# Kernel tuning notes

Hardware: AMD Instinct MI355X
Metric: run time of the kernel (lower is better)

The kernel has to match this reference:

```python
import jax, jax.numpy as jnp
import numpy as np

N = 100000
E = 1600000
DIN = 165
DH = 128


def setup_inputs() -> dict:
    key = jax.random.key(0)
    ks = jax.random.split(key, 10)
    def nrm(k, shape, scale=0.1):
        return jax.random.normal(k, shape, dtype=jnp.float32) * scale
    x = jax.random.normal(ks[0], (N, DIN), dtype=jnp.float32)
    edge_index = jax.random.randint(ks[1], (2, E), 0, N, dtype=jnp.int64)
    return dict(
        x=x,
        edge_index=edge_index,
        fb_w1=nrm(ks[2], (DIN, DIN // 2)),
        fb_w2=nrm(ks[3], (DIN // 2, DIN)),
        sage_wl=nrm(ks[4], (DIN, DH)),
        sage_bl=jnp.zeros((DH,), jnp.float32),
        sage_wr=nrm(ks[5], (DIN, DH)),
        gat_w=nrm(ks[6], (DH, DH // 2)),
        gat_att_src=nrm(ks[7], (DH // 2,)),
        gat_att_dst=nrm(ks[8], (DH // 2,)),
        gat_b=jnp.zeros((DH // 2,), jnp.float32),
        cheb_w=nrm(ks[9], (DH // 2, 1)),
        cheb_b=jnp.zeros((1,), jnp.float32),
    )


def _segment_softmax(logits, seg, num_segments):
    mx = jax.ops.segment_max(logits, seg, num_segments=num_segments)
    e = jnp.exp(logits - mx[seg])
    s = jax.ops.segment_sum(e, seg, num_segments=num_segments)
    return e / (s[seg] + 1e-16)


def reference(x, edge_index, fb_w1, fb_w2, sage_wl, sage_bl, sage_wr,
              gat_w, gat_att_src, gat_att_dst, gat_b, cheb_w, cheb_b):
    n = x.shape[0]
    src, dst = edge_index[0], edge_index[1]

    # FeatureBooster: scatter over batch=arange(n) is identity for max and sum,
    # so max_result == sum_result == x and y = sigmoid(mlp(x) + mlp(x)).
    m = jnp.maximum(x @ fb_w1, 0.0) @ fb_w2
    x = x * jax.nn.sigmoid(m + m)

    # SAGEConv (mean aggregation): out = lin_l(mean_agg(x_src -> dst)) + lin_r(x)
    agg = jax.ops.segment_sum(x[src], dst, num_segments=n)  # [n, DIN]
    cnt = jax.ops.segment_sum(jnp.ones((src.shape[0],), x.dtype), dst, num_segments=n)
    agg = agg / jnp.maximum(cnt, 1.0)[:, None]
    x = agg @ sage_wl + sage_bl + x @ sage_wr
    x = jnp.maximum(x, 0.0)  # relu; dropout is identity in eval mode

    # GATConv (heads=1) with default add_self_loops=True
    ar = jnp.arange(n, dtype=src.dtype)
    si = jnp.concatenate([src, ar])
    di = jnp.concatenate([dst, ar])
    h = x @ gat_w                      # [n, 64]
    a_s = h @ gat_att_src              # [n]
    a_d = h @ gat_att_dst              # [n]
    e = a_s[si] + a_d[di]
    e = jnp.where(e > 0, e, 0.2 * e)   # leaky_relu slope 0.2
    alpha = _segment_softmax(e, di, n)
    x = jax.ops.segment_sum(h[si] * alpha[:, None], di, num_segments=n) + gat_b
    x = jnp.maximum(x, 0.0)

    # ChebConv with K=1: T_0(x) = x, so it's a plain linear layer.
    x = x @ cheb_w + cheb_b
    return jax.nn.sigmoid(x)
```

## Files before the change

kernel.cpp:

```cpp
#include <hip/hip_runtime.h>
#include <hip/hip_bf16.h>

#define N_NODES 100000
#define N_EDGES 1600000
#define DIN 165
#define DHID 82
#define DH 128
#define DG 64

typedef _Float16 f16;
typedef f16 f16x8 __attribute__((ext_vector_type(8)));
typedef f16 f16x4 __attribute__((ext_vector_type(4)));
typedef f16 f16x2 __attribute__((ext_vector_type(2)));
typedef float f32x4 __attribute__((ext_vector_type(4)));

#define MFMA16(a, b, c) __builtin_amdgcn_mfma_f32_16x16x32_f16(a, b, c, 0, 0, 0)


__global__ __launch_bounds__(256) void rank_xpad_kernel(const float* __restrict__ x,
                                                        f16* __restrict__ Xp,
                                                        const int* __restrict__ dst,
                                                        int* __restrict__ cnt,
                                                        int* __restrict__ rank) {
    int gid = blockIdx.x * 256 + threadIdx.x;
    if (gid < N_EDGES) rank[gid] = atomicAdd(&cnt[dst[gid]], 1);
    int node = gid / 48, g = gid % 48;
    int col0 = g * 4;
    f16x4 o;
#pragma unroll
    for (int j = 0; j < 4; j++) {
        int c = col0 + j;
        o[j] = (f16)((c < DIN) ? x[(long)node * DIN + c] : 0.f);
    }
    *((f16x4*)(Xp + (long)node * 192 + col0)) = o;
}

__global__ __launch_bounds__(1024) void scan1_kernel(const int* __restrict__ cnt,
                                                     int* __restrict__ rowptr,
                                                     int* __restrict__ bsum) {
    __shared__ int wsum[16];
    int tid = threadIdx.x, lane = tid & 63, wid = tid >> 6;
    int i = blockIdx.x * 1024 + tid;
    int v = (i < N_NODES) ? cnt[i] : 0;
    int xv = v;
#pragma unroll
    for (int off = 1; off < 64; off <<= 1) {
        int t = __shfl_up(xv, off);
        if (lane >= off) xv += t;
    }
    if (lane == 63) wsum[wid] = xv;
    __syncthreads();
    if (wid == 0 && lane < 16) {
        int wv = wsum[lane];
#pragma unroll
        for (int off = 1; off < 16; off <<= 1) {
            int t = __shfl_up(wv, off);
            if (lane >= off) wv += t;
        }
        wsum[lane] = wv;
    }
    __syncthreads();
    int off0 = wid ? wsum[wid - 1] : 0;
    if (i < N_NODES) rowptr[i] = off0 + xv - v;
    if (tid == 1023) bsum[blockIdx.x] = off0 + xv;
}

__global__ __launch_bounds__(64) void scan2_kernel(const int* __restrict__ bsum,
                                                   int* __restrict__ boff,
                                                   int* __restrict__ rowptr,
                                                   int nblocks) {
    int lane = threadIdx.x;
    int c = 0;
    for (int base = 0; base < nblocks; base += 64) {
        int idx = base + lane;
        int v = (idx < nblocks) ? bsum[idx] : 0;
        int xv = v;
#pragma unroll
        for (int off = 1; off < 64; off <<= 1) {
            int t = __shfl_up(xv, off);
            if (lane >= off) xv += t;
        }
        if (idx < nblocks) boff[idx] = c + xv - v;
        c += __shfl(xv, 63);
    }
    if (lane == 0) rowptr[N_NODES] = c;
}

__global__ __launch_bounds__(1024) void scan3_kernel(int* __restrict__ rowptr,
                                                     const int* __restrict__ boff) {
    int i = blockIdx.x * 1024 + threadIdx.x;
    if (i < N_NODES) rowptr[i] += boff[blockIdx.x];
}

__global__ __launch_bounds__(256) void h_fill_kernel(const f16* __restrict__ Xp,
                                                     const float* __restrict__ w1,
                                                     f16* __restrict__ H,
                                                     const int* __restrict__ src,
                                                     const int* __restrict__ dst,
                                                     const int* __restrict__ rank,
                                                     const int* __restrict__ rowptr,
                                                     int* __restrict__ esrc) {
    int tid = threadIdx.x, wave = tid >> 6, lane = tid & 63;
    {
        int tg = blockIdx.x * 256 + tid;
        for (int e = tg; e < N_EDGES; e += 384 * 256) {
            int d = dst[e];
            __builtin_nontemporal_store(src[e], &esrc[rowptr[d] + rank[e]]);
        }
    }
    int q = lane >> 4, l16 = lane & 15;
    int blk = blockIdx.x;
    int g = (blk >> 3) & 1;
    int chunk = (blk & 7) + 8 * (blk >> 4);
    int nbase = g * 48;
    f16x8 bf[3][6];
#pragma unroll
    for (int nt = 0; nt < 3; nt++) {
        int col = nbase + nt * 16 + l16;
#pragma unroll
        for (int ks = 0; ks < 6; ks++) {
            int kb = ks * 32 + q * 8;
            f16x8 b;
#pragma unroll
            for (int j = 0; j < 8; j++) {
                int k = kb + j;
                b[j] = (f16)((k < DIN && col < DHID) ? w1[k * DHID + col] : 0.f);
            }
            bf[nt][ks] = b;
        }
    }
    for (int mt = chunk * 4 + wave; mt < 6250; mt += 768) {
        const f16* xr = Xp + (long)(mt * 16 + l16) * 192;
        f32x4 acc[3];
#pragma unroll
        for (int nt = 0; nt < 3; nt++) acc[nt] = (f32x4){0.f, 0.f, 0.f, 0.f};
#pragma unroll
        for (int ks = 0; ks < 6; ks++) {
            f16x8 a = *((const f16x8*)(xr + ks * 32 + q * 8));
#pragma unroll
            for (int nt = 0; nt < 3; nt++) acc[nt] = MFMA16(a, bf[nt][ks], acc[nt]);
        }
#pragma unroll
        for (int nt = 0; nt < 3; nt++) {
            int col = nbase + nt * 16 + l16;
#pragma unroll
            for (int r = 0; r < 4; r++) {
                int node = mt * 16 + q * 4 + r;
                H[(long)node * 96 + col] = (f16)fmaxf(acc[nt][r], 0.f);
            }
        }
    }
}

__global__ __launch_bounds__(256) void y_kernel(const f16* __restrict__ Xp,
                                                const f16* __restrict__ H,
                                                const float* __restrict__ w2,
                                                f16* __restrict__ Y) {
    int tid = threadIdx.x, wave = tid >> 6, lane = tid & 63;
    int q = lane >> 4, l16 = lane & 15;
    int blk = blockIdx.x;
    int g = (blk >> 3) & 3;
    int chunk = (blk & 7) + 8 * (blk >> 5);
    int nbase = g * 48;
    f16x8 bf[3][3];
#pragma unroll
    for (int nt = 0; nt < 3; nt++) {
        int col = nbase + nt * 16 + l16;
#pragma unroll
        for (int ks = 0; ks < 3; ks++) {
            int kb = ks * 32 + q * 8;
            f16x8 b;
#pragma unroll
            for (int j = 0; j < 8; j++) {
                int k = kb + j;
                b[j] = (f16)((k < DHID && col < DIN) ? w2[k * DIN + col] : 0.f);
            }
            bf[nt][ks] = b;
        }
    }
    for (int mt = chunk * 4 + wave; mt < 6250; mt += 768) {
        const f16* hr = H + (long)(mt * 16 + l16) * 96;
        f32x4 acc[3];
#pragma unroll
        for (int nt = 0; nt < 3; nt++) acc[nt] = (f32x4){0.f, 0.f, 0.f, 0.f};
#pragma unroll
        for (int ks = 0; ks < 3; ks++) {
            f16x8 a = *((const f16x8*)(hr + ks * 32 + q * 8));
#pragma unroll
            for (int nt = 0; nt < 3; nt++) acc[nt] = MFMA16(a, bf[nt][ks], acc[nt]);
        }
#pragma unroll
        for (int nt = 0; nt < 3; nt++) {
            int col = nbase + nt * 16 + l16;
#pragma unroll
            for (int r = 0; r < 4; r++) {
                int node = mt * 16 + q * 4 + r;
                float gg = 1.f / (1.f + __expf(-2.f * acc[nt][r]));
                float xv = (float)Xp[(long)node * 192 + col];
                Y[(long)node * 192 + col] = (f16)(xv * gg);
            }
        }
    }
}

__global__ __launch_bounds__(256) void sage_lin_kernel(const f16* __restrict__ Y,
                                                       const float* __restrict__ wl,
                                                       const float* __restrict__ wr,
                                                       const float* __restrict__ bl,
                                                       f16* __restrict__ t_l,
                                                       f16* __restrict__ x2) {
    int tid = threadIdx.x, wave = tid >> 6, lane = tid & 63;
    int q = lane >> 4, l16 = lane & 15;
    int blk = blockIdx.x;
    int g = (blk >> 3) & 3;
    int chunk = (blk & 7) + 8 * (blk >> 5);
    bool isR = (g >= 2);
    const float* W = isR ? wr : wl;
    int cbase = (g & 1) * 64;
    f16x8 bf[4][6];
    float blv[4];
#pragma unroll
    for (int nt = 0; nt < 4; nt++) {
        int col = cbase + nt * 16 + l16;
        blv[nt] = isR ? bl[col] : 0.f;
#pragma unroll
        for (int ks = 0; ks < 6; ks++) {
            int kb = ks * 32 + q * 8;
            f16x8 b;
#pragma unroll
            for (int j = 0; j < 8; j++) {
                int k = kb + j;
                b[j] = (f16)((k < DIN) ? W[k * DH + col] : 0.f);
            }
            bf[nt][ks] = b;
        }
    }
    for (int mt = chunk * 4 + wave; mt < 6250; mt += 768) {
        const f16* yrow = Y + (long)(mt * 16 + l16) * 192;
        f32x4 acc[4];
#pragma unroll
        for (int nt = 0; nt < 4; nt++) acc[nt] = (f32x4){0.f, 0.f, 0.f, 0.f};
#pragma unroll
        for (int ks = 0; ks < 6; ks++) {
            f16x8 a = *((const f16x8*)(yrow + ks * 32 + q * 8));
#pragma unroll
            for (int nt = 0; nt < 4; nt++) acc[nt] = MFMA16(a, bf[nt][ks], acc[nt]);
        }
#pragma unroll
        for (int nt = 0; nt < 4; nt++) {
            int col = cbase + nt * 16 + l16;
#pragma unroll
            for (int r = 0; r < 4; r++) {
                int node = mt * 16 + q * 4 + r;
                if (isR)
                    x2[(long)node * DH + col] = (f16)(acc[nt][r] + blv[nt]);
                else
                    t_l[(long)node * DH + col] = (f16)acc[nt][r];
            }
        }
    }
}

__global__ __launch_bounds__(256) void sage_agg_kernel(const f16* __restrict__ t_l,
                                                       const int* __restrict__ rowptr,
                                                       const int* __restrict__ esrc,
                                                       f16* __restrict__ x2) {
    int wid = threadIdx.x >> 6, lane = threadIdx.x & 63;
    int i = blockIdx.x * 4 + wid;
    int r0 = rowptr[i], r1 = rowptr[i + 1];
    int quarter = lane >> 4, fq = lane & 15;
    float acc[8];
#pragma unroll
    for (int k = 0; k < 8; k++) acc[k] = 0.f;
    for (int e0 = r0; e0 < r1; e0 += 64) {
        int cnt = min(64, r1 - e0);
        int sn_v = (lane < cnt) ? esrc[e0 + lane] : 0;
        int jmax = (cnt + 3) >> 2;
        for (int j = 0; j < jmax; j++) {
            int idx = 4 * j + quarter;
            int sn = __shfl(sn_v, idx);
            float v = (idx < cnt) ? 1.f : 0.f;
            f16x8 p = *((const f16x8*)(t_l + ((long)sn << 7) + fq * 8));
#pragma unroll
            for (int k = 0; k < 8; k++) acc[k] = fmaf(v, (float)p[k], acc[k]);
        }
    }
#pragma unroll
    for (int k = 0; k < 8; k++) {
        acc[k] += __shfl_xor(acc[k], 16);
        acc[k] += __shfl_xor(acc[k], 32);
    }
    if (quarter == 0) {
        float inv = 1.f / fmaxf((float)(r1 - r0), 1.f);
        f16x8* xp = (f16x8*)(x2 + (long)i * DH + fq * 8);
        f16x8 pre = *xp;
        f16x8 o;
#pragma unroll
        for (int k = 0; k < 8; k++) o[k] = (f16)fmaxf((float)pre[k] + acc[k] * inv, 0.f);
        *xp = o;
    }
}

__global__ __launch_bounds__(256) void gat_h_kernel(const f16* __restrict__ x2,
                                                    const float* __restrict__ gw,
                                                    const float* __restrict__ att_s_w,
                                                    const float* __restrict__ att_d_w,
                                                    f16* __restrict__ h,
                                                    float* __restrict__ a_s,
                                                    float* __restrict__ a_d) {
    int tid = threadIdx.x, wave = tid >> 6, lane = tid & 63;
    int q = lane >> 4, l16 = lane & 15;
    f16x8 bf[4][4];
    float asw[4], adw[4];
#pragma unroll
    for (int nt = 0; nt < 4; nt++) {
        int col = nt * 16 + l16;
        asw[nt] = att_s_w[col];
        adw[nt] = att_d_w[col];
#pragma unroll
        for (int ks = 0; ks < 4; ks++) {
            int kb = ks * 32 + q * 8;
            f16x8 b;
#pragma unroll
            for (int j = 0; j < 8; j++) b[j] = (f16)gw[(kb + j) * DG + col];
            bf[nt][ks] = b;
        }
    }
    int stride = gridDim.x * 4;
    for (int mt = blockIdx.x * 4 + wave; mt < 6250; mt += stride) {
        const f16* xr = x2 + (long)(mt * 16 + l16) * DH;
        f32x4 acc[4];
#pragma unroll
        for (int nt = 0; nt < 4; nt++) acc[nt] = (f32x4){0.f, 0.f, 0.f, 0.f};
#pragma unroll
        for (int ks = 0; ks < 4; ks++) {
            f16x8 a = *((const f16x8*)(xr + ks * 32 + q * 8));
#pragma unroll
            for (int nt = 0; nt < 4; nt++) acc[nt] = MFMA16(a, bf[nt][ks], acc[nt]);
        }
#pragma unroll
        for (int r = 0; r < 4; r++) {
            int node = mt * 16 + q * 4 + r;
            float vs = 0.f, vd = 0.f;
#pragma unroll
            for (int nt = 0; nt < 4; nt++) {
                float hv = acc[nt][r];
                h[(long)node * DG + nt * 16 + l16] = (f16)hv;
                vs += hv * asw[nt];
                vd += hv * adw[nt];
            }
#pragma unroll
            for (int off = 1; off < 16; off <<= 1) {
                vs += __shfl_xor(vs, off);
                vd += __shfl_xor(vd, off);
            }
            if (l16 == 0) {
                a_s[node] = vs;
                a_d[node] = vd;
            }
        }
    }
}

__device__ __forceinline__ float leaky02(float v) { return v > 0.f ? v : 0.2f * v; }

__global__ __launch_bounds__(256) void gat_agg_kernel(const f16* __restrict__ h,
                                                      const float* __restrict__ a_s,
                                                      const float* __restrict__ a_d,
                                                      const int* __restrict__ rowptr,
                                                      const int* __restrict__ esrc,
                                                      const float* __restrict__ gat_b,
                                                      const float* __restrict__ cheb_w,
                                                      const float* __restrict__ cheb_b,
                                                      float* __restrict__ out) {
    int wid = threadIdx.x >> 6, lane = threadIdx.x & 63;
    int i = blockIdx.x * 4 + wid;
    int r0 = rowptr[i], r1 = rowptr[i + 1];
    int quarter = lane >> 4, fq = lane & 15;
    float adi = a_d[i];
    float acc[4] = {0.f, 0.f, 0.f, 0.f};
    float sv = 0.f;
    for (int e0 = r0; e0 < r1; e0 += 64) {
        int cnt = min(64, r1 - e0);
        int sn_v = (lane < cnt) ? esrc[e0 + lane] : 0;
        float ev = 0.f;
        if (lane < cnt) ev = __expf(leaky02(a_s[sn_v] + adi));
        sv += ev;
        int jmax = (cnt + 3) >> 2;
        for (int j = 0; j < jmax; j++) {
            int idx = 4 * j + quarter;
            int sn = __shfl(sn_v, idx);
            float w = __shfl(ev, idx);
            f16x4 p = *((const f16x4*)(h + ((long)sn << 6) + fq * 4));
#pragma unroll
            for (int k = 0; k < 4; k++) acc[k] = fmaf(w, (float)p[k], acc[k]);
        }
    }
#pragma unroll
    for (int off = 32; off > 0; off >>= 1) sv += __shfl_xor(sv, off);
#pragma unroll
    for (int k = 0; k < 4; k++) {
        acc[k] += __shfl_xor(acc[k], 16);
        acc[k] += __shfl_xor(acc[k], 32);
    }
    if (quarter == 0) {
        float wself = __expf(leaky02(a_s[i] + adi));
        float s = sv + wself;
        f16x4 ph = *((const f16x4*)(h + ((long)i << 6) + fq * 4));
        float4 gb = ((const float4*)gat_b)[fq];
        float4 cw = ((const float4*)cheb_w)[fq];
        float gbv[4] = {gb.x, gb.y, gb.z, gb.w};
        float cwv[4] = {cw.x, cw.y, cw.z, cw.w};
        float inv = 1.f / s;
        float z = 0.f;
#pragma unroll
        for (int k = 0; k < 4; k++) {
            float o = fmaxf(fmaf(wself, (float)ph[k], acc[k]) * inv + gbv[k], 0.f);
            z = fmaf(o, cwv[k], z);
        }
#pragma unroll
        for (int off = 8; off > 0; off >>= 1) z += __shfl_xor(z, off);
        if (fq == 0) out[i] = 1.f / (1.f + __expf(-(z + cheb_b[0])));
    }
}

extern "C" void kernel_launch(void* const* d_in, const int* in_sizes, int n_in,
                              void* d_out, int out_size, void* d_ws, size_t ws_size,
                              hipStream_t stream) {
    const float* x       = (const float*)d_in[0];
    const int*   eidx    = (const int*)d_in[1];
    const float* fb_w1   = (const float*)d_in[2];
    const float* fb_w2   = (const float*)d_in[3];
    const float* sage_wl = (const float*)d_in[4];
    const float* sage_bl = (const float*)d_in[5];
    const float* sage_wr = (const float*)d_in[6];
    const float* gat_w   = (const float*)d_in[7];
    const float* att_src = (const float*)d_in[8];
    const float* att_dst = (const float*)d_in[9];
    const float* gat_b   = (const float*)d_in[10];
    const float* cheb_w  = (const float*)d_in[11];
    const float* cheb_b  = (const float*)d_in[12];

    const int* src = eidx;
    const int* dst = eidx + N_EDGES;

    char* base = (char*)d_ws;
    f16* Xp = (f16*)base;
    f16* H  = (f16*)(base + 38400000);
    f16* Y  = (f16*)(base + 57600000);
    f16* t_l = (f16*)base;
    f16* x2  = (f16*)(base + 25600000);
    f16* h   = Y;
    float* a_s = (float*)(base + 70400000);
    float* a_d = a_s + N_NODES;
    int* rowptr = (int*)(base + 96000000);
    int* cnt  = rowptr + (N_NODES + 1);
    int* esrc = cnt + N_NODES;
    int* rank = esrc + N_EDGES;
    int* bsum = rank + N_EDGES;
    int* boff = bsum + 128;

    const int SCAN_BLOCKS = (N_NODES + 1023) / 1024;

    hipMemsetAsync(cnt, 0, N_NODES * sizeof(int), stream);

    rank_xpad_kernel<<<(N_NODES * 48) / 256, 256, 0, stream>>>(x, Xp, dst, cnt, rank);
    scan1_kernel<<<SCAN_BLOCKS, 1024, 0, stream>>>(cnt, rowptr, bsum);
    scan2_kernel<<<1, 64, 0, stream>>>(bsum, boff, rowptr, SCAN_BLOCKS);
    scan3_kernel<<<SCAN_BLOCKS, 1024, 0, stream>>>(rowptr, boff);
    h_fill_kernel<<<384, 256, 0, stream>>>(Xp, fb_w1, H, src, dst, rank, rowptr, esrc);
    y_kernel<<<768, 256, 0, stream>>>(Xp, H, fb_w2, Y);
    sage_lin_kernel<<<768, 256, 0, stream>>>(Y, sage_wl, sage_wr, sage_bl, t_l, x2);
    sage_agg_kernel<<<N_NODES / 4, 256, 0, stream>>>(t_l, rowptr, esrc, x2);
    gat_h_kernel<<<392, 256, 0, stream>>>(x2, gat_w, att_src, att_dst, h, a_s, a_d);
    gat_agg_kernel<<<N_NODES / 4, 256, 0, stream>>>(h, a_s, a_d, rowptr, esrc, gat_b,
                                                    cheb_w, cheb_b, (float*)d_out);
}
```

Before: 484.5 us.

## Fuse front-end kernels into one cooperative persistent kernel with grid syncs

Replaces the first seven launches (rank/pad, three-stage scan, H fill, Y, SAGE linear) with a single cooperative kernel of 512 blocks that separates phases with grid-wide syncs. The scan is reorganised into 256-wide blocks with a single-block middle pass. It aims to remove launch gaps and tail effects between small kernels, at the cost of grid-sync overhead and fixed occupancy. If the cooperative launch fails, the old multi-kernel path runs.

```diff
diff --git a/kernel.cpp b/kernel.cpp
--- a/kernel.cpp
+++ b/kernel.cpp
@@ -1,5 +1,8 @@
 #include <hip/hip_runtime.h>
 #include <hip/hip_bf16.h>
+#include <hip/hip_cooperative_groups.h>
+
+namespace cg = cooperative_groups;
 
 #define N_NODES 100000
 #define N_EDGES 1600000
@@ -16,6 +19,268 @@
 
 #define MFMA16(a, b, c) __builtin_amdgcn_mfma_f32_16x16x32_f16(a, b, c, 0, 0, 0)
 
+
+struct MegaArgs {
+    const float* x;
+    const int* dst;
+    const int* src;
+    const float* w1;
+    const float* w2;
+    const float* wl;
+    const float* wr;
+    const float* bl;
+    f16* Xp;
+    f16* H;
+    f16* Y;
+    f16* t_l;
+    f16* x2;
+    int* cnt;
+    int* rank;
+    int* rowptr;
+    int* bsum;
+    int* boff;
+    int* esrc;
+};
+
+#define GSYNC() do { __threadfence(); grid.sync(); __threadfence(); } while (0)
+
+__global__ __launch_bounds__(256, 2) void mega_kernel(MegaArgs a) {
+    cg::grid_group grid = cg::this_grid();
+    int tid = threadIdx.x, blk = blockIdx.x;
+    int wave = tid >> 6, lane = tid & 63;
+    int q = lane >> 4, l16 = lane & 15;
+
+    if (blk < 256) {
+        for (int e = blk * 256 + tid; e < N_EDGES; e += 256 * 256)
+            a.rank[e] = atomicAdd(&a.cnt[a.dst[e]], 1);
+    } else {
+        for (int gid = (blk - 256) * 256 + tid; gid < N_NODES * 48; gid += 256 * 256) {
+            int node = gid / 48, g = gid % 48;
+            int col0 = g * 4;
+            f16x4 o;
+#pragma unroll
+            for (int j = 0; j < 4; j++) {
+                int c = col0 + j;
+                o[j] = (f16)((c < DIN) ? a.x[(long)node * DIN + c] : 0.f);
+            }
+            *((f16x4*)(a.Xp + (long)node * 192 + col0)) = o;
+        }
+    }
+    GSYNC();
+
+    {
+        __shared__ int wsum[4];
+        int i = blk * 256 + tid;
+        int v = (i < N_NODES) ? a.cnt[i] : 0;
+        int xv = v;
+#pragma unroll
+        for (int off = 1; off < 64; off <<= 1) {
+            int t = __shfl_up(xv, off);
+            if (lane >= off) xv += t;
+        }
+        if (lane == 63) wsum[wave] = xv;
+        __syncthreads();
+        if (wave == 0 && lane < 4) {
+            int wv = wsum[lane];
+#pragma unroll
+            for (int off = 1; off < 4; off <<= 1) {
+                int t = __shfl_up(wv, off);
+                if (lane >= off) wv += t;
+            }
+            wsum[lane] = wv;
+        }
+        __syncthreads();
+        int off0 = wave ? wsum[wave - 1] : 0;
+        if (i <= N_NODES) a.rowptr[i] = off0 + xv - v;
+        if (tid == 255) a.bsum[blk] = off0 + xv;
+    }
+    GSYNC();
+
+    if (blk == 0) {
+        __shared__ int ws2[4];
+        __shared__ int carry_s;
+        if (tid == 0) carry_s = 0;
+        __syncthreads();
+        for (int c0 = 0; c0 < 512; c0 += 256) {
+            int idx = c0 + tid;
+            int v = a.bsum[idx];
+            int xv = v;
+#pragma unroll
+            for (int off = 1; off < 64; off <<= 1) {
+                int t = __shfl_up(xv, off);
+                if (lane >= off) xv += t;
+            }
+            if (lane == 63) ws2[wave] = xv;
+            __syncthreads();
+            if (wave == 0 && lane < 4) {
+                int wv = ws2[lane];
+#pragma unroll
+                for (int off = 1; off < 4; off <<= 1) {
+                    int t = __shfl_up(wv, off);
+                    if (lane >= off) wv += t;
+                }
+                ws2[lane] = wv;
+            }
+            __syncthreads();
+            int off0 = (wave ? ws2[wave - 1] : 0) + carry_s;
+            a.boff[idx] = off0 + xv - v;
+            __syncthreads();
+            if (tid == 0) carry_s += ws2[3];
+            __syncthreads();
+        }
+    }
+    GSYNC();
+
+    {
+        int i = blk * 256 + tid;
+        if (i <= N_NODES) a.rowptr[i] += a.boff[i >> 8];
+    }
+    GSYNC();
+
+    for (int e = blk * 256 + tid; e < N_EDGES; e += 512 * 256) {
+        int d = a.dst[e];
+        __builtin_nontemporal_store(a.src[e], &a.esrc[a.rowptr[d] + a.rank[e]]);
+    }
+    {
+        int g = (blk >> 3) & 1;
+        int chunk = (blk & 7) + 8 * (blk >> 4);
+        int nbase = g * 48;
+        f16x8 bf[3][6];
+#pragma unroll
+        for (int nt = 0; nt < 3; nt++) {
+            int col = nbase + nt * 16 + l16;
+#pragma unroll
+            for (int ks = 0; ks < 6; ks++) {
+                int kb = ks * 32 + q * 8;
+                f16x8 b;
+#pragma unroll
+                for (int j = 0; j < 8; j++) {
+                    int k = kb + j;
+                    b[j] = (f16)((k < DIN && col < DHID) ? a.w1[k * DHID + col] : 0.f);
+                }
+                bf[nt][ks] = b;
+            }
+        }
+        for (int mt = chunk * 4 + wave; mt < 6250; mt += 1024) {
+            const f16* xr = a.Xp + (long)(mt * 16 + l16) * 192;
+            f32x4 acc[3];
+#pragma unroll
+            for (int nt = 0; nt < 3; nt++) acc[nt] = (f32x4){0.f, 0.f, 0.f, 0.f};
+#pragma unroll
+            for (int ks = 0; ks < 6; ks++) {
+                f16x8 av = *((const f16x8*)(xr + ks * 32 + q * 8));
+#pragma unroll
+                for (int nt = 0; nt < 3; nt++) acc[nt] = MFMA16(av, bf[nt][ks], acc[nt]);
+            }
+#pragma unroll
+            for (int nt = 0; nt < 3; nt++) {
+                int col = nbase + nt * 16 + l16;
+#pragma unroll
+                for (int r = 0; r < 4; r++) {
+                    int node = mt * 16 + q * 4 + r;
+                    a.H[(long)node * 96 + col] = (f16)fmaxf(acc[nt][r], 0.f);
+                }
+            }
+        }
+    }
+    GSYNC();
+
+    {
+        int g = (blk >> 3) & 3;
+        int chunk = (blk & 7) + 8 * (blk >> 5);
+        int nbase = g * 48;
+        f16x8 bf[3][3];
+#pragma unroll
+        for (int nt = 0; nt < 3; nt++) {
+            int col = nbase + nt * 16 + l16;
+#pragma unroll
+            for (int ks = 0; ks < 3; ks++) {
+                int kb = ks * 32 + q * 8;
+                f16x8 b;
+#pragma unroll
+                for (int j = 0; j < 8; j++) {
+                    int k = kb + j;
+                    b[j] = (f16)((k < DHID && col < DIN) ? a.w2[k * DIN + col] : 0.f);
+                }
+                bf[nt][ks] = b;
+            }
+        }
+        for (int mt = chunk * 4 + wave; mt < 6250; mt += 512) {
+            const f16* hr = a.H + (long)(mt * 16 + l16) * 96;
+            f32x4 acc[3];
+#pragma unroll
+            for (int nt = 0; nt < 3; nt++) acc[nt] = (f32x4){0.f, 0.f, 0.f, 0.f};
+#pragma unroll
+            for (int ks = 0; ks < 3; ks++) {
+                f16x8 av = *((const f16x8*)(hr + ks * 32 + q * 8));
+#pragma unroll
+                for (int nt = 0; nt < 3; nt++) acc[nt] = MFMA16(av, bf[nt][ks], acc[nt]);
+            }
+#pragma unroll
+            for (int nt = 0; nt < 3; nt++) {
+                int col = nbase + nt * 16 + l16;
+#pragma unroll
+                for (int r = 0; r < 4; r++) {
+                    int node = mt * 16 + q * 4 + r;
+                    float gg = 1.f / (1.f + __expf(-2.f * acc[nt][r]));
+                    float xv = (float)a.Xp[(long)node * 192 + col];
+                    a.Y[(long)node * 192 + col] = (f16)(xv * gg);
+                }
+            }
+        }
+    }
+    GSYNC();
+
+    {
+        int g = (blk >> 3) & 3;
+        int chunk = (blk & 7) + 8 * (blk >> 5);
+        bool isR = (g >= 2);
+        const float* W = isR ? a.wr : a.wl;
+        int cbase = (g & 1) * 64;
+        f16x8 bf[4][6];
+        float blv[4];
+#pragma unroll
+        for (int nt = 0; nt < 4; nt++) {
+            int col = cbase + nt * 16 + l16;
+            blv[nt] = isR ? a.bl[col] : 0.f;
+#pragma unroll
+            for (int ks = 0; ks < 6; ks++) {
+                int kb = ks * 32 + q * 8;
+                f16x8 b;
+#pragma unroll
+                for (int j = 0; j < 8; j++) {
+                    int k = kb + j;
+                    b[j] = (f16)((k < DIN) ? W[k * DH + col] : 0.f);
+                }
+                bf[nt][ks] = b;
+            }
+        }
+        for (int mt = chunk * 4 + wave; mt < 6250; mt += 512) {
+            const f16* yrow = a.Y + (long)(mt * 16 + l16) * 192;
+            f32x4 acc[4];
+#pragma unroll
+            for (int nt = 0; nt < 4; nt++) acc[nt] = (f32x4){0.f, 0.f, 0.f, 0.f};
+#pragma unroll
+            for (int ks = 0; ks < 6; ks++) {
+                f16x8 av = *((const f16x8*)(yrow + ks * 32 + q * 8));
+#pragma unroll
+                for (int nt = 0; nt < 4; nt++) acc[nt] = MFMA16(av, bf[nt][ks], acc[nt]);
+            }
+#pragma unroll
+            for (int nt = 0; nt < 4; nt++) {
+                int col = cbase + nt * 16 + l16;
+#pragma unroll
+                for (int r = 0; r < 4; r++) {
+                    int node = mt * 16 + q * 4 + r;
+                    if (isR)
+                        a.x2[(long)node * DH + col] = (f16)(acc[nt][r] + blv[nt]);
+                    else
+                        a.t_l[(long)node * DH + col] = (f16)acc[nt][r];
+                }
+            }
+        }
+    }
+}
 
 __global__ __launch_bounds__(256) void rank_xpad_kernel(const float* __restrict__ x,
                                                         f16* __restrict__ Xp,
@@ -458,19 +723,27 @@
     int* esrc = cnt + N_NODES;
     int* rank = esrc + N_EDGES;
     int* bsum = rank + N_EDGES;
-    int* boff = bsum + 128;
-
-    const int SCAN_BLOCKS = (N_NODES + 1023) / 1024;
+    int* boff = bsum + 768;
 
     hipMemsetAsync(cnt, 0, N_NODES * sizeof(int), stream);
 
-    rank_xpad_kernel<<<(N_NODES * 48) / 256, 256, 0, stream>>>(x, Xp, dst, cnt, rank);
-    scan1_kernel<<<SCAN_BLOCKS, 1024, 0, stream>>>(cnt, rowptr, bsum);
-    scan2_kernel<<<1, 64, 0, stream>>>(bsum, boff, rowptr, SCAN_BLOCKS);
-    scan3_kernel<<<SCAN_BLOCKS, 1024, 0, stream>>>(rowptr, boff);
-    h_fill_kernel<<<384, 256, 0, stream>>>(Xp, fb_w1, H, src, dst, rank, rowptr, esrc);
-    y_kernel<<<768, 256, 0, stream>>>(Xp, H, fb_w2, Y);
-    sage_lin_kernel<<<768, 256, 0, stream>>>(Y, sage_wl, sage_wr, sage_bl, t_l, x2);
+    MegaArgs margs = {x, dst, src, fb_w1, fb_w2, sage_wl, sage_wr, sage_bl,
+                      Xp, H, Y, t_l, x2, cnt, rank, rowptr, bsum, boff, esrc};
+    void* kargs[] = {(void*)&margs};
+    hipError_t cerr = hipLaunchCooperativeKernel((const void*)mega_kernel, dim3(512),
+                                                 dim3(256), kargs, 0, stream);
+    if (cerr != hipSuccess) {
+        const int SCAN_BLOCKS = (N_NODES + 1023) / 1024;
+        hipMemsetAsync(cnt, 0, N_NODES * sizeof(int), stream);
+        rank_xpad_kernel<<<(N_NODES * 48) / 256, 256, 0, stream>>>(x, Xp, dst, cnt, rank);
+        scan1_kernel<<<SCAN_BLOCKS, 1024, 0, stream>>>(cnt, rowptr, bsum);
+        scan2_kernel<<<1, 64, 0, stream>>>(bsum, boff, rowptr, SCAN_BLOCKS);
+        scan3_kernel<<<SCAN_BLOCKS, 1024, 0, stream>>>(rowptr, boff);
+        h_fill_kernel<<<384, 256, 0, stream>>>(Xp, fb_w1, H, src, dst, rank, rowptr, esrc);
+        y_kernel<<<768, 256, 0, stream>>>(Xp, H, fb_w2, Y);
+        sage_lin_kernel<<<768, 256, 0, stream>>>(Y, sage_wl, sage_wr, sage_bl, t_l, x2);
+    }
+
     sage_agg_kernel<<<N_NODES / 4, 256, 0, stream>>>(t_l, rowptr, esrc, x2);
     gat_h_kernel<<<392, 256, 0, stream>>>(x2, gat_w, att_src, att_dst, h, a_s, a_d);
     gat_agg_kernel<<<N_NODES / 4, 256, 0, stream>>>(h, a_s, a_d, rowptr, esrc, gat_b,
```

New measurement: 1.357 ms. +180.1%, slower.

## Fuse three-pass scan into one kernel and defer block offsets to consumers

Applied to the files above, without the earlier changes.

The three scan launches are replaced by one scan kernel. The last block to arrive, detected with an atomic counter, scans the per-block sums into boff. The block-offset add is dropped from rowptr: h_fill, sage_agg and gat_agg now add boff[i>>10] when they read rowptr. rank_xpad_kernel also gives edge-ranking and x-padding separate blocks, interleaved 1 in 4, instead of mixing both jobs in each thread. This removes two small launches and a full rowptr rewrite, at the cost of an extra boff lookup in every consumer and reliance on threadfence and atomic ordering across blocks.

```diff
diff --git a/kernel.cpp b/kernel.cpp
--- a/kernel.cpp
+++ b/kernel.cpp
@@ -22,25 +22,35 @@
                                                         const int* __restrict__ dst,
                                                         int* __restrict__ cnt,
                                                         int* __restrict__ rank) {
-    int gid = blockIdx.x * 256 + threadIdx.x;
-    if (gid < N_EDGES) rank[gid] = atomicAdd(&cnt[dst[gid]], 1);
-    int node = gid / 48, g = gid % 48;
-    int col0 = g * 4;
-    f16x4 o;
-#pragma unroll
-    for (int j = 0; j < 4; j++) {
-        int c = col0 + j;
-        o[j] = (f16)((c < DIN) ? x[(long)node * DIN + c] : 0.f);
-    }
-    *((f16x4*)(Xp + (long)node * 192 + col0)) = o;
-}
-
-__global__ __launch_bounds__(1024) void scan1_kernel(const int* __restrict__ cnt,
-                                                     int* __restrict__ rowptr,
-                                                     int* __restrict__ bsum) {
+    int blk = blockIdx.x, tid = threadIdx.x;
+    if ((blk & 3) == 0) {
+        int e = (blk >> 2) * 256 + tid;
+        rank[e] = atomicAdd(&cnt[dst[e]], 1);
+    } else {
+        int xb = blk - (blk >> 2) - 1;
+        int gid = xb * 256 + tid;
+        int node = gid / 48, g = gid % 48;
+        int col0 = g * 4;
+        f16x4 o;
+#pragma unroll
+        for (int j = 0; j < 4; j++) {
+            int c = col0 + j;
+            o[j] = (f16)((c < DIN) ? x[(long)node * DIN + c] : 0.f);
+        }
+        *((f16x4*)(Xp + (long)node * 192 + col0)) = o;
+    }
+}
+
+__global__ __launch_bounds__(1024) void scan_kernel(const int* __restrict__ cnt,
+                                                    int* __restrict__ rowptr,
+                                                    int* __restrict__ bsum,
+                                                    int* __restrict__ boff,
+                                                    int* __restrict__ arrived) {
     __shared__ int wsum[16];
+    __shared__ int lastflag;
     int tid = threadIdx.x, lane = tid & 63, wid = tid >> 6;
-    int i = blockIdx.x * 1024 + tid;
+    int blk = blockIdx.x;
+    int i = blk * 1024 + tid;
     int v = (i < N_NODES) ? cnt[i] : 0;
     int xv = v;
 #pragma unroll
@@ -61,35 +71,33 @@
     }
     __syncthreads();
     int off0 = wid ? wsum[wid - 1] : 0;
-    if (i < N_NODES) rowptr[i] = off0 + xv - v;
-    if (tid == 1023) bsum[blockIdx.x] = off0 + xv;
-}
-
-__global__ __launch_bounds__(64) void scan2_kernel(const int* __restrict__ bsum,
-                                                   int* __restrict__ boff,
-                                                   int* __restrict__ rowptr,
-                                                   int nblocks) {
-    int lane = threadIdx.x;
-    int c = 0;
-    for (int base = 0; base < nblocks; base += 64) {
-        int idx = base + lane;
-        int v = (idx < nblocks) ? bsum[idx] : 0;
-        int xv = v;
-#pragma unroll
-        for (int off = 1; off < 64; off <<= 1) {
-            int t = __shfl_up(xv, off);
-            if (lane >= off) xv += t;
-        }
-        if (idx < nblocks) boff[idx] = c + xv - v;
-        c += __shfl(xv, 63);
-    }
-    if (lane == 0) rowptr[N_NODES] = c;
-}
-
-__global__ __launch_bounds__(1024) void scan3_kernel(int* __restrict__ rowptr,
-                                                     const int* __restrict__ boff) {
-    int i = blockIdx.x * 1024 + threadIdx.x;
-    if (i < N_NODES) rowptr[i] += boff[blockIdx.x];
+    if (i <= N_NODES) rowptr[i] = off0 + xv - v;
+    if (tid == 1023) bsum[blk] = off0 + xv;
+    __threadfence();
+    if (tid == 0) {
+        int old = atomicAdd(arrived, 1);
+        lastflag = (old == 97);
+    }
+    __syncthreads();
+    if (lastflag && wid == 0) {
+        __threadfence();
+        int c = 0;
+        for (int base = 0; base < 98; base += 64) {
+            int idx = base + lane;
+            int bv = 0;
+            if (idx < 98)
+                bv = __hip_atomic_load(&bsum[idx], __ATOMIC_RELAXED,
+                                       __HIP_MEMORY_SCOPE_AGENT);
+            int sv = bv;
+#pragma unroll
+            for (int off = 1; off < 64; off <<= 1) {
+                int t = __shfl_up(sv, off);
+                if (lane >= off) sv += t;
+            }
+            if (idx < 98) boff[idx] = c + sv - bv;
+            c += __shfl(sv, 63);
+        }
+    }
 }
 
 __global__ __launch_bounds__(256) void h_fill_kernel(const f16* __restrict__ Xp,
@@ -99,13 +107,14 @@
                                                      const int* __restrict__ dst,
                                                      const int* __restrict__ rank,
                                                      const int* __restrict__ rowptr,
+                                                     const int* __restrict__ boff,
                                                      int* __restrict__ esrc) {
     int tid = threadIdx.x, wave = tid >> 6, lane = tid & 63;
     {
         int tg = blockIdx.x * 256 + tid;
         for (int e = tg; e < N_EDGES; e += 384 * 256) {
             int d = dst[e];
-            __builtin_nontemporal_store(src[e], &esrc[rowptr[d] + rank[e]]);
+            __builtin_nontemporal_store(src[e], &esrc[rowptr[d] + boff[d >> 10] + rank[e]]);
         }
     }
     int q = lane >> 4, l16 = lane & 15;
@@ -263,11 +272,13 @@
 
 __global__ __launch_bounds__(256) void sage_agg_kernel(const f16* __restrict__ t_l,
                                                        const int* __restrict__ rowptr,
+                                                       const int* __restrict__ boff,
                                                        const int* __restrict__ esrc,
                                                        f16* __restrict__ x2) {
     int wid = threadIdx.x >> 6, lane = threadIdx.x & 63;
     int i = blockIdx.x * 4 + wid;
-    int r0 = rowptr[i], r1 = rowptr[i + 1];
+    int r0 = rowptr[i] + boff[i >> 10];
+    int r1 = rowptr[i + 1] + boff[(i + 1) >> 10];
     int quarter = lane >> 4, fq = lane & 15;
     float acc[8];
 #pragma unroll
@@ -368,6 +379,7 @@
                                                       const float* __restrict__ a_s,
                                                       const float* __restrict__ a_d,
                                                       const int* __restrict__ rowptr,
+                                                      const int* __restrict__ boff,
                                                       const int* __restrict__ esrc,
                                                       const float* __restrict__ gat_b,
                                                       const float* __restrict__ cheb_w,
@@ -375,7 +387,8 @@
                                                       float* __restrict__ out) {
     int wid = threadIdx.x >> 6, lane = threadIdx.x & 63;
     int i = blockIdx.x * 4 + wid;
-    int r0 = rowptr[i], r1 = rowptr[i + 1];
+    int r0 = rowptr[i] + boff[i >> 10];
+    int r1 = rowptr[i + 1] + boff[(i + 1) >> 10];
     int quarter = lane >> 4, fq = lane & 15;
     float adi = a_d[i];
     float acc[4] = {0.f, 0.f, 0.f, 0.f};
@@ -453,26 +466,23 @@
     f16* h   = Y;
     float* a_s = (float*)(base + 70400000);
     float* a_d = a_s + N_NODES;
-    int* rowptr = (int*)(base + 96000000);
-    int* cnt  = rowptr + (N_NODES + 1);
-    int* esrc = cnt + N_NODES;
-    int* rank = esrc + N_EDGES;
-    int* bsum = rank + N_EDGES;
-    int* boff = bsum + 128;
-
-    const int SCAN_BLOCKS = (N_NODES + 1023) / 1024;
-
-    hipMemsetAsync(cnt, 0, N_NODES * sizeof(int), stream);
-
-    rank_xpad_kernel<<<(N_NODES * 48) / 256, 256, 0, stream>>>(x, Xp, dst, cnt, rank);
-    scan1_kernel<<<SCAN_BLOCKS, 1024, 0, stream>>>(cnt, rowptr, bsum);
-    scan2_kernel<<<1, 64, 0, stream>>>(bsum, boff, rowptr, SCAN_BLOCKS);
-    scan3_kernel<<<SCAN_BLOCKS, 1024, 0, stream>>>(rowptr, boff);
-    h_fill_kernel<<<384, 256, 0, stream>>>(Xp, fb_w1, H, src, dst, rank, rowptr, esrc);
+    int* rowptr  = (int*)(base + 96000000);
+    int* cnt     = rowptr + (N_NODES + 1);
+    int* arrived = cnt + N_NODES;
+    int* esrc    = arrived + 1;
+    int* rank    = esrc + N_EDGES;
+    int* bsum    = rank + N_EDGES;
+    int* boff    = bsum + 128;
+
+    hipMemsetAsync(cnt, 0, (N_NODES + 1) * sizeof(int), stream);
+
+    rank_xpad_kernel<<<25000, 256, 0, stream>>>(x, Xp, dst, cnt, rank);
+    scan_kernel<<<98, 1024, 0, stream>>>(cnt, rowptr, bsum, boff, arrived);
+    h_fill_kernel<<<384, 256, 0, stream>>>(Xp, fb_w1, H, src, dst, rank, rowptr, boff, esrc);
     y_kernel<<<768, 256, 0, stream>>>(Xp, H, fb_w2, Y);
     sage_lin_kernel<<<768, 256, 0, stream>>>(Y, sage_wl, sage_wr, sage_bl, t_l, x2);
-    sage_agg_kernel<<<N_NODES / 4, 256, 0, stream>>>(t_l, rowptr, esrc, x2);
+    sage_agg_kernel<<<N_NODES / 4, 256, 0, stream>>>(t_l, rowptr, boff, esrc, x2);
     gat_h_kernel<<<392, 256, 0, stream>>>(x2, gat_w, att_src, att_dst, h, a_s, a_d);
-    gat_agg_kernel<<<N_NODES / 4, 256, 0, stream>>>(h, a_s, a_d, rowptr, esrc, gat_b,
+    gat_agg_kernel<<<N_NODES / 4, 256, 0, stream>>>(h, a_s, a_d, rowptr, boff, esrc, gat_b,
                                                     cheb_w, cheb_b, (float*)d_out);
 }
```

New measurement: 492.1 us. About the same (+1.6%).
